# Kernel optimization log

Measured on AMD Instinct MI355X. Metric: run time of the kernel, lower is better.

## Reference

```python
import jax, jax.numpy as jnp
import numpy as np

HD = 256          # hidden_dim[0]
KF = 2            # k factor
KD = HD * KF      # 512, bilinear feature dim
L = 2000          # hard-coded sequence length
B = 4
NEG = np.float32(np.finfo(np.float32).min)  # finite min, NOT -inf (matches torch code)
EPS = 1e-5


def _fc(x, V, g, b):
    # weight_norm(Linear, dim=None): W = g * V / ||V||_F, then ReLU
    W = (g / jnp.linalg.norm(V)) * V  # [KD, HD]
    return jax.nn.relu(jnp.einsum('blh,kh->blk', x, W) + b)


def setup_inputs() -> dict:
    key = jax.random.key(0)
    ks = jax.random.split(key, 12)
    X = jax.random.normal(ks[0], (B, L, HD), dtype=jnp.float32)
    Y = jax.random.normal(ks[1], (B, L, HD), dtype=jnp.float32)
    mask1 = jax.random.bernoulli(ks[2], 0.8, (B, L)).astype(jnp.float32)
    mask2 = jax.random.bernoulli(ks[3], 0.8, (B, L)).astype(jnp.float32)
    # Q_net / K_net params (single weight-normed linear each)
    Qv = jax.random.normal(ks[4], (KD, HD), dtype=jnp.float32) * 0.05
    Qg = jnp.asarray(1.0, dtype=jnp.float32)
    Qb = jax.random.normal(ks[5], (KD,), dtype=jnp.float32) * 0.05
    Kv = jax.random.normal(ks[6], (KD, HD), dtype=jnp.float32) * 0.05
    Kg = jnp.asarray(1.0, dtype=jnp.float32)
    Kb = jax.random.normal(ks[7], (KD,), dtype=jnp.float32) * 0.05
    h_mat = jax.random.normal(ks[8], (KD,), dtype=jnp.float32)   # (1,1,KD) squeezed
    h_bias = jax.random.normal(ks[9], (), dtype=jnp.float32)     # (1,1,1) squeezed
    gamma = jnp.ones((KD,), dtype=jnp.float32)                   # BatchNorm1d affine
    beta = jnp.zeros((KD,), dtype=jnp.float32)
    return {"X": X, "Y": Y, "mask1": mask1, "mask2": mask2,
            "Qv": Qv, "Qg": Qg, "Qb": Qb, "Kv": Kv, "Kg": Kg, "Kb": Kb,
            "h_mat": h_mat, "h_bias": h_bias, "gamma": gamma, "beta": beta}


def _masked_softmax(A, m_row):
    # m_row: [B,1,L], broadcasts over axis 1; softmax over dim 1 as in torch
    logits = jnp.where(m_row > 0, A, NEG)
    att = jax.nn.softmax(logits, axis=1)
    return m_row * att


def reference(X, Y, mask1, mask2, Qv, Qg, Qb, Kv, Kg, Kb, h_mat, h_bias, gamma, beta):
    A1_X = _fc(X, Qv, Qg, Qb)  # [B,L,KD]
    A1_Y = _fc(Y, Kv, Kg, Kb)
    A2_Y = _fc(Y, Qv, Qg, Qb)
    A2_X = _fc(X, Kv, Kg, Kb)
    # bilinear co-attention maps [B,L,L]
    A1 = jnp.einsum('bvk,bqk->bvq', A1_X * h_mat, A1_Y) + h_bias
    A2 = jnp.einsum('bqk,bvk->bqv', A2_Y * h_mat, A2_X) + h_bias
    m1r = mask1[:, None, :]  # mask1_attend[b,v,q] = mask1[b,q]
    m2r = mask2[:, None, :]
    alpha = _masked_softmax(A1, m2r)
    logits_X = jnp.einsum('bvq,bqk->bvk', alpha, A1_Y) * mask1[:, :, None]
    beta_att = _masked_softmax(A2, m1r)
    logits_Y = jnp.einsum('bqv,bvk->bqk', beta_att, A2_X) * mask2[:, :, None]
    # AvgPool2d((2000,1)) == mean over sequence dim
    pooled = logits_X.mean(axis=1) + logits_Y.mean(axis=1)  # [B,KD]
    # BatchNorm1d training-mode forward (biased batch stats)
    mu = pooled.mean(axis=0)
    var = pooled.var(axis=0)
    return gamma * (pooled - mu) * jax.lax.rsqrt(var + EPS) + beta
```

## Files before the change

### kernel.cpp

```cpp
#include <hip/hip_runtime.h>

#define NB 4
#define LSEQ 2000
#define HD 256
#define KD 512
#define LPAD 2048
#define SMALL_N 18562

using short8 = __attribute__((ext_vector_type(8))) short;
using f32x4  = __attribute__((ext_vector_type(4))) float;
typedef unsigned short u16;

__device__ __forceinline__ float b2f(u16 u) { return __uint_as_float(((unsigned)u) << 16); }
__device__ __forceinline__ u16 f2b(float f) {
    unsigned u = __float_as_uint(f);
    u += 0x7FFFu + ((u >> 16) & 1u);
    return (u16)(u >> 16);
}
__device__ __forceinline__ bool detect32(const void* gamma) {
    return ((const float*)gamma)[0] == 1.0f;
}
__device__ __forceinline__ void gl_lds16(const u16* g, short* l) {
    __builtin_amdgcn_global_load_lds(
        (const __attribute__((address_space(1))) unsigned int*)g,
        (__attribute__((address_space(3))) unsigned int*)l, 16, 0, 0);
}

__global__ void convert_kernel(const void* X, const void* Y, const void* Qv, const void* Kv,
                               const void* m1, const void* m2, const void* Qb, const void* Kb,
                               const void* hm, const void* Qg, const void* Kg,
                               const void* gamma, const void* beta,
                               u16* __restrict__ Xb, u16* __restrict__ Yb,
                               u16* __restrict__ Qvb, u16* __restrict__ Kvb,
                               float* __restrict__ smallf, float* __restrict__ ssq)
{
    const bool is32 = detect32(gamma);
    const int seg = blockIdx.y;
    if (seg < 4) {
        const void* src = seg == 0 ? X : seg == 1 ? Y : seg == 2 ? Qv : Kv;
        u16* dst = seg == 0 ? Xb : seg == 1 ? Yb : seg == 2 ? Qvb : Kvb;
        const int n = (seg < 2) ? NB * LSEQ * HD : KD * HD;
        const int i0 = (blockIdx.x * 256 + threadIdx.x) * 8;
        if (i0 >= n) return;
        uint4 pack;
        u16* v = (u16*)&pack;
        if (is32) {
            float4 fa = ((const float4*)src)[(i0 >> 2)];
            float4 fb = ((const float4*)src)[(i0 >> 2) + 1];
            v[0] = f2b(fa.x); v[1] = f2b(fa.y); v[2] = f2b(fa.z); v[3] = f2b(fa.w);
            v[4] = f2b(fb.x); v[5] = f2b(fb.y); v[6] = f2b(fb.z); v[7] = f2b(fb.w);
        } else {
            pack = ((const uint4*)src)[i0 >> 3];
        }
        ((uint4*)dst)[i0 >> 3] = pack;
        if (seg >= 2) {
            float s = 0.f;
            #pragma unroll
            for (int j = 0; j < 8; ++j) { float f = b2f(v[j]); s = fmaf(f, f, s); }
            #pragma unroll
            for (int off = 32; off > 0; off >>= 1) s += __shfl_xor(s, off);
            if ((threadIdx.x & 63) == 0) atomicAdd(&ssq[seg - 2], s);
        }
    } else {
        const int i0 = (blockIdx.x * 256 + threadIdx.x) * 4;
        for (int i = i0; i < i0 + 4; ++i) {
            if (i >= SMALL_N) break;
            const void* src; int off;
            if      (i <  8000) { src = m1;    off = i; }
            else if (i < 16000) { src = m2;    off = i - 8000; }
            else if (i < 16512) { src = Qb;    off = i - 16000; }
            else if (i < 17024) { src = Kb;    off = i - 16512; }
            else if (i < 17536) { src = hm;    off = i - 17024; }
            else if (i < 18048) { src = gamma; off = i - 17536; }
            else if (i < 18560) { src = beta;  off = i - 18048; }
            else if (i == 18560) {
                float f = ((const float*)Qg)[0];
                smallf[i] = (f == 1.0f) ? 1.0f : b2f(((const u16*)Qg)[0]);
                continue;
            } else {
                float f = ((const float*)Kg)[0];
                smallf[i] = (f == 1.0f) ? 1.0f : b2f(((const u16*)Kg)[0]);
                continue;
            }
            smallf[i] = is32 ? ((const float*)src)[off] : b2f(((const u16*)src)[off]);
        }
    }
}

__global__ __launch_bounds__(256, 2)
void fc_kernel(const u16* __restrict__ X, const u16* __restrict__ Y,
               const u16* __restrict__ Qv, const u16* __restrict__ Kv,
               const float* __restrict__ Qbf, const float* __restrict__ Kbf,
               const float* __restrict__ hf, const float* __restrict__ gv,
               const float* __restrict__ ssq, u16* __restrict__ fc)
{
    const int mt = blockIdx.x, nt = blockIdx.y, t = blockIdx.z;
    const int b = t >> 2, which = t & 3;
    const u16* In = ((which == 0) | (which == 3)) ? (X + (size_t)b * LSEQ * HD)
                                                  : (Y + (size_t)b * LSEQ * HD);
    const bool isQ = (which == 0) | (which == 2);
    const u16* W      = isQ ? Qv : Kv;
    const float* bias = isQ ? Qbf : Kbf;
    const int j = isQ ? 0 : 1;
    const float s = gv[j] / sqrtf(ssq[j]);
    u16* out = fc + (size_t)t * LSEQ * KD;

    __shared__ __align__(16) short As[2][128 * 32];
    __shared__ __align__(16) short Bs[2][128 * 32];

    const int tid = threadIdx.x;
    const int lane = tid & 63, wave = tid >> 6;
    const int wm = wave >> 1, wn = wave & 1;
    const int quad = lane >> 4, l15 = lane & 15;
    const int sr = tid >> 2, sc = tid & 3;
    const int scz = sc ^ ((sr >> 1) & 3);
    const int m0 = mt * 128, n0 = nt * 128;

    int gm0 = min(m0 + sr, LSEQ - 1), gm1 = min(m0 + sr + 64, LSEQ - 1);
    const u16* pA0 = In + (size_t)gm0 * HD + scz * 8;
    const u16* pA1 = In + (size_t)gm1 * HD + scz * 8;
    const u16* pB0 = W + (size_t)(n0 + sr) * HD + scz * 8;
    const u16* pB1 = W + (size_t)(n0 + sr + 64) * HD + scz * 8;
    const int dof = sr * 32 + sc * 8;

    int aoff[4], boff[4];
    #pragma unroll
    for (int i = 0; i < 4; ++i) {
        int ra = wm * 64 + i * 16 + l15;
        aoff[i] = ra * 32 + (quad ^ ((ra >> 1) & 3)) * 8;
        int rb = wn * 64 + i * 16 + l15;
        boff[i] = rb * 32 + (quad ^ ((rb >> 1) & 3)) * 8;
    }

    gl_lds16(pA0, &As[0][dof]);
    gl_lds16(pA1, &As[0][64 * 32 + dof]);
    gl_lds16(pB0, &Bs[0][dof]);
    gl_lds16(pB1, &Bs[0][64 * 32 + dof]);
    __syncthreads();

    f32x4 acc[4][4] = {};

    for (int kt = 0; kt < 8; ++kt) {
        const int cur = kt & 1, nxt = cur ^ 1;
        if (kt < 7) {
            const int ko = (kt + 1) * 32;
            gl_lds16(pA0 + ko, &As[nxt][dof]);
            gl_lds16(pA1 + ko, &As[nxt][64 * 32 + dof]);
            gl_lds16(pB0 + ko, &Bs[nxt][dof]);
            gl_lds16(pB1 + ko, &Bs[nxt][64 * 32 + dof]);
        }
        short8 af[4], bf[4];
        #pragma unroll
        for (int i = 0; i < 4; ++i) af[i] = *(const short8*)&As[cur][aoff[i]];
        #pragma unroll
        for (int i = 0; i < 4; ++i) bf[i] = *(const short8*)&Bs[cur][boff[i]];
        #pragma unroll
        for (int mi = 0; mi < 4; ++mi)
            #pragma unroll
            for (int ni = 0; ni < 4; ++ni)
                acc[mi][ni] = __builtin_amdgcn_mfma_f32_16x16x32_bf16(af[mi], bf[ni], acc[mi][ni], 0, 0, 0);
        __syncthreads();
    }

    #pragma unroll
    for (int ni = 0; ni < 4; ++ni) {
        int n = n0 + wn * 64 + ni * 16 + l15;
        float bv = bias[n];
        float hv = isQ ? hf[n] : 1.0f;
        #pragma unroll
        for (int mi = 0; mi < 4; ++mi) {
            int mb = m0 + wm * 64 + mi * 16 + quad * 4;
            #pragma unroll
            for (int r = 0; r < 4; ++r) {
                int m = mb + r;
                if (m < LSEQ) {
                    float v = fmaf(s, acc[mi][ni][r], bv);
                    v = v > 0.f ? v : 0.f;
                    out[(size_t)m * KD + n] = f2b(v * hv);
                }
            }
        }
    }
}

__global__ __launch_bounds__(512, 2)
void colsm_kernel(const u16* __restrict__ fc, const float* __restrict__ m1f,
                  const float* __restrict__ m2f,
                  float* __restrict__ part_d, float* __restrict__ part_n)
{
    const int n_lin = blockIdx.x + 8 * blockIdx.y + 64 * blockIdx.z;
    const int xcd = n_lin & 7, slot = n_lin >> 3;
    const int pvs = xcd & 3, gqt = xcd >> 2;
    const int inner = slot & 7;
    const int vs = 2 * pvs + (inner & 1);
    const int qt = 4 * gqt + (inner >> 1);
    const int z  = slot >> 3;
    const int a = z >> 2, b = z & 3;
    const u16* R  = fc + (size_t)(b * 4 + (a == 0 ? 1 : 3)) * LSEQ * KD;
    const u16* Sm = fc + (size_t)(b * 4 + (a == 0 ? 0 : 2)) * LSEQ * KD;
    const float* wmask = (a == 0 ? m1f : m2f) + (size_t)b * LSEQ;

    __shared__ __align__(16) short AL[4][256 * 32];
    __shared__ __align__(16) short BL[4][256 * 32];

    const int tid = threadIdx.x;
    const int lane = tid & 63, wave = tid >> 6;
    const int wm = wave >> 2, wn = wave & 3;
    const int quad = lane >> 4, l15 = lane & 15;
    const int r0 = qt * 256, c0 = vs * 256;

    const int srow = tid >> 2;
    const int kslot = (tid & 3) ^ ((tid >> 3) & 3);
    int grA0 = min(r0 + srow, LSEQ - 1), grA1 = min(r0 + 128 + srow, LSEQ - 1);
    int gcB0 = min(c0 + srow, LSEQ - 1), gcB1 = min(c0 + 128 + srow, LSEQ - 1);
    const u16* pRa = R  + (size_t)grA0 * KD + kslot * 8;
    const u16* pRb = R  + (size_t)grA1 * KD + kslot * 8;
    const u16* pSa = Sm + (size_t)gcB0 * KD + kslot * 8;
    const u16* pSb = Sm + (size_t)gcB1 * KD + kslot * 8;
    const int ldst = tid * 8;

    const int swz = (quad ^ ((l15 >> 1) & 3)) * 8;

    #define STAGE_A(h) { short* d_ = &AL[(h) & 3][ldst];               \
                         gl_lds16(pRa + (h) * 32, d_);                 \
                         gl_lds16(pRb + (h) * 32, d_ + 4096); }
    #define STAGE_B(h) { short* d_ = &BL[(h) & 3][ldst];               \
                         gl_lds16(pSa + (h) * 32, d_);                 \
                         gl_lds16(pSb + (h) * 32, d_ + 4096); }

    STAGE_A(0); STAGE_B(0); STAGE_A(1); STAGE_B(1); STAGE_A(2); STAGE_B(2);
    asm volatile("s_waitcnt vmcnt(4)" ::: "memory");
    __builtin_amdgcn_s_barrier();
    __builtin_amdgcn_sched_barrier(0);

    f32x4 acc[8][4] = {};
    short8 bf[4];

    #pragma unroll 2
    for (int t = 0; t < 8; ++t) {
        #pragma unroll
        for (int p = 0; p < 4; ++p) {
            const int j = 2 * t + (p >> 1);
            const short* Ab = AL[j & 3];
            const short* Bb = BL[j & 3];
            short8 af[4];
            #pragma unroll
            for (int mi = 0; mi < 4; ++mi) {
                int lr = wm * 128 + (p & 1) * 64 + mi * 16 + l15;
                af[mi] = *(const short8*)&Ab[lr * 32 + swz];
            }
            if ((p & 1) == 0) {
                #pragma unroll
                for (int ni = 0; ni < 4; ++ni) {
                    int lc = wn * 64 + ni * 16 + l15;
                    bf[ni] = *(const short8*)&Bb[lc * 32 + swz];
                }
            }
            if (p == 0)      { if (2 * t + 3 <= 15) STAGE_A(2 * t + 3); }
            else if (p == 1) { if (2 * t + 3 <= 15) STAGE_B(2 * t + 3); }
            else if (p == 2) { if (2 * t + 4 <= 15) STAGE_A(2 * t + 4); }
            else {
                if (2 * t + 4 <= 15) STAGE_B(2 * t + 4);
                if (t < 6)       asm volatile("s_waitcnt vmcnt(4)" ::: "memory");
                else if (t == 6) asm volatile("s_waitcnt vmcnt(0)" ::: "memory");
            }
            asm volatile("" ::: "memory");
            __builtin_amdgcn_s_barrier();
            __builtin_amdgcn_sched_barrier(0);
            __builtin_amdgcn_s_setprio(1);
            #pragma unroll
            for (int mi = 0; mi < 4; ++mi)
                #pragma unroll
                for (int ni = 0; ni < 4; ++ni)
                    acc[(p & 1) * 4 + mi][ni] =
                        __builtin_amdgcn_mfma_f32_16x16x32_bf16(af[mi], bf[ni],
                                                                acc[(p & 1) * 4 + mi][ni], 0, 0, 0);
            __builtin_amdgcn_s_setprio(0);
            asm volatile("" ::: "memory");
            __builtin_amdgcn_s_barrier();
            __builtin_amdgcn_sched_barrier(0);
        }
    }

    __syncthreads();
    float* ldsD = (float*)&AL[0][0];
    float* ldsN = (float*)&AL[1][0];

    float wv[4], vv[4];
    #pragma unroll
    for (int ni = 0; ni < 4; ++ni) {
        int cg = c0 + wn * 64 + ni * 16 + l15;
        bool valid = cg < LSEQ;
        vv[ni] = valid ? 1.f : 0.f;
        wv[ni] = valid ? wmask[min(cg, LSEQ - 1)] : 0.f;
    }
    #pragma unroll
    for (int aq = 0; aq < 8; ++aq)
        #pragma unroll
        for (int r = 0; r < 4; ++r) {
            float d = 0.f, n = 0.f;
            #pragma unroll
            for (int ni = 0; ni < 4; ++ni) {
                float e = __expf(acc[aq][ni][r]);
                d = fmaf(vv[ni], e, d);
                n = fmaf(wv[ni], e, n);
            }
            #pragma unroll
            for (int off = 1; off < 16; off <<= 1) {
                d += __shfl_xor(d, off);
                n += __shfl_xor(n, off);
            }
            if (l15 == 0) {
                int row = wm * 128 + (aq >> 2) * 64 + (aq & 3) * 16 + quad * 4 + r;
                ldsD[row * 4 + wn] = d;
                ldsN[row * 4 + wn] = n;
            }
        }
    __syncthreads();
    if (tid < 256) {
        int q = r0 + tid;
        if (q < LSEQ) {
            size_t p = ((size_t)(z * 8 + vs)) * LPAD + q;
            part_d[p] = ldsD[tid * 4 + 0] + ldsD[tid * 4 + 1] + ldsD[tid * 4 + 2] + ldsD[tid * 4 + 3];
            part_n[p] = ldsN[tid * 4 + 0] + ldsN[tid * 4 + 1] + ldsN[tid * 4 + 2] + ldsN[tid * 4 + 3];
        }
    }
    #undef STAGE_A
    #undef STAGE_B
}

__global__ void combine_kernel(const float* __restrict__ part_d, const float* __restrict__ part_n,
                               const float* __restrict__ m1f, const float* __restrict__ m2f,
                               float* __restrict__ c, float* __restrict__ pooled)
{
    int idx = blockIdx.x * 256 + threadIdx.x;
    if (idx < NB * KD) pooled[idx] = 0.f;
    int z = idx >> 11, q = idx & (LPAD - 1);
    int a = z >> 2, b = z & 3;
    float d = 0.f, n = 0.f;
    #pragma unroll
    for (int vs = 0; vs < 8; ++vs) {
        size_t p = ((size_t)(z * 8 + vs)) * LPAD + q;
        d += part_d[p]; n += part_n[p];
    }
    float val = 0.f;
    if (q < LSEQ) {
        float om = (a == 0 ? m2f : m1f)[b * LSEQ + q];
        val = om * n / d;
    }
    c[(size_t)z * LPAD + q] = val;
}

__global__ void pooled_kernel(const u16* __restrict__ fc, const float* __restrict__ c,
                              float* __restrict__ pooled)
{
    const int b = blockIdx.x, rs = blockIdx.y;
    const int k = threadIdx.x;
    const u16* YK = fc + (size_t)(b * 4 + 1) * LSEQ * KD;
    const u16* XK = fc + (size_t)(b * 4 + 3) * LSEQ * KD;
    const float* c1 = c + (size_t)(0 + b) * LPAD;
    const float* c2 = c + (size_t)(4 + b) * LPAD;
    float s = 0.f;
    const int rbeg = rs * 50, rend = rbeg + 50;
    for (int r = rbeg; r < rend; ++r) {
        s = fmaf(c1[r], b2f(YK[(size_t)r * KD + k]), s);
        s = fmaf(c2[r], b2f(XK[(size_t)r * KD + k]), s);
    }
    atomicAdd(&pooled[b * KD + k], s * (1.0f / LSEQ));
}

__global__ void ln_kernel(const float* __restrict__ pooled, const float* __restrict__ gammaf,
                          const float* __restrict__ betaf, const void* __restrict__ gamma_orig,
                          void* __restrict__ out)
{
    int k = blockIdx.x * 256 + threadIdx.x;
    float p[NB];
    #pragma unroll
    for (int b = 0; b < NB; ++b) p[b] = pooled[b * KD + k];
    float mu = 0.25f * (p[0] + p[1] + p[2] + p[3]);
    float var = 0.f;
    #pragma unroll
    for (int b = 0; b < NB; ++b) { float d = p[b] - mu; var = fmaf(d, d, var); }
    var *= 0.25f;
    float inv = rsqrtf(var + 1e-5f);
    float g = gammaf[k], be = betaf[k];
    const bool is32 = detect32(gamma_orig);
    #pragma unroll
    for (int b = 0; b < NB; ++b) {
        float v = fmaf(g * (p[b] - mu), inv, be);
        if (is32) ((float*)out)[b * KD + k] = v;
        else      ((u16*)out)[b * KD + k] = f2b(v);
    }
}

extern "C" void kernel_launch(void* const* d_in, const int* in_sizes, int n_in,
                              void* d_out, int out_size, void* d_ws, size_t ws_size,
                              hipStream_t stream)
{
    const void* X  = d_in[0];
    const void* Y  = d_in[1];
    const void* m1 = d_in[2];
    const void* m2 = d_in[3];
    const void* Qv = d_in[4];
    const void* Qg = d_in[5];
    const void* Qb = d_in[6];
    const void* Kv = d_in[7];
    const void* Kg = d_in[8];
    const void* Kb = d_in[9];
    const void* h  = d_in[10];
    const void* gamma = d_in[12];
    const void* beta  = d_in[13];

    char* ws = (char*)d_ws;
    size_t off = 0;
    u16* Xb  = (u16*)(ws + off); off += (size_t)NB * LSEQ * HD * 2;
    u16* Yb  = (u16*)(ws + off); off += (size_t)NB * LSEQ * HD * 2;
    u16* Qvb = (u16*)(ws + off); off += (size_t)KD * HD * 2;
    u16* Kvb = (u16*)(ws + off); off += (size_t)KD * HD * 2;
    float* smallf = (float*)(ws + off); off += ((size_t)(SMALL_N + 2) * 4 + 15) / 16 * 16;
    u16* fc  = (u16*)(ws + off); off += (size_t)16 * LSEQ * KD * 2;
    float* part_d = (float*)(ws + off); off += (size_t)8 * 8 * LPAD * 4;
    float* part_n = (float*)(ws + off); off += (size_t)8 * 8 * LPAD * 4;
    float* c      = (float*)(ws + off); off += (size_t)8 * LPAD * 4;
    float* pooled = (float*)(ws + off); off += (size_t)NB * KD * 4;

    const float* m1f = smallf;
    const float* m2f = smallf + 8000;
    const float* Qbf = smallf + 16000;
    const float* Kbf = smallf + 16512;
    const float* hf  = smallf + 17024;
    const float* gmf = smallf + 17536;
    const float* bef = smallf + 18048;
    const float* gv  = smallf + 18560;
    float* ssq = smallf + SMALL_N;

    hipMemsetAsync(ssq, 0, 2 * sizeof(float), stream);
    convert_kernel<<<dim3(1000, 5), 256, 0, stream>>>(X, Y, Qv, Kv, m1, m2, Qb, Kb, h, Qg, Kg,
                                                      gamma, beta, Xb, Yb, Qvb, Kvb, smallf, ssq);
    fc_kernel     <<<dim3(16, 4, 16), 256, 0, stream>>>(Xb, Yb, Qvb, Kvb, Qbf, Kbf, hf, gv, ssq, fc);
    colsm_kernel  <<<dim3(8, 8, 8), 512, 0, stream>>>(fc, m1f, m2f, part_d, part_n);
    combine_kernel<<<64, 256, 0, stream>>>(part_d, part_n, m1f, m2f, c, pooled);
    pooled_kernel <<<dim3(4, 40), 512, 0, stream>>>(fc, c, pooled);
    ln_kernel     <<<2, 256, 0, stream>>>(pooled, gmf, bef, gamma, d_out);
}
```

Before: 188.5 us.

## Shrink colsm LDS ring to double buffer and raise occupancy bound

Replaces the 4-deep LDS staging ring and its hand-scheduled vmcnt waits and split barriers with a plain double buffer. Each iteration prefetches the next K slice and ends with a __syncthreads. Softmax reduction scratch moves to its own small shared arrays, and launch bounds rise from 2 to 4 blocks. The aim is to cut LDS use so more blocks fit per CU and latency is hidden by occupancy instead of deep prefetch. In exchange the register cap tightens a lot against a 128-float accumulator, which risks spills, and each step now pays a full barrier with a shallower prefetch.

```diff
diff --git a/kernel.cpp b/kernel.cpp
--- a/kernel.cpp
+++ b/kernel.cpp
@@ -183,7 +183,7 @@
     }
 }
 
-__global__ __launch_bounds__(512, 2)
+__global__ __launch_bounds__(512, 4)
 void colsm_kernel(const u16* __restrict__ fc, const float* __restrict__ m1f,
                   const float* __restrict__ m2f,
                   float* __restrict__ part_d, float* __restrict__ part_n)
@@ -200,8 +200,10 @@
     const u16* Sm = fc + (size_t)(b * 4 + (a == 0 ? 0 : 2)) * LSEQ * KD;
     const float* wmask = (a == 0 ? m1f : m2f) + (size_t)b * LSEQ;
 
-    __shared__ __align__(16) short AL[4][256 * 32];
-    __shared__ __align__(16) short BL[4][256 * 32];
+    __shared__ __align__(16) short AL[2][256 * 32];
+    __shared__ __align__(16) short BL[2][256 * 32];
+    __shared__ float ldsD[256][4];
+    __shared__ float ldsN[256][4];
 
     const int tid = threadIdx.x;
     const int lane = tid & 63, wave = tid >> 6;
@@ -218,73 +220,51 @@
     const u16* pSa = Sm + (size_t)gcB0 * KD + kslot * 8;
     const u16* pSb = Sm + (size_t)gcB1 * KD + kslot * 8;
     const int ldst = tid * 8;
-
     const int swz = (quad ^ ((l15 >> 1) & 3)) * 8;
 
-    #define STAGE_A(h) { short* d_ = &AL[(h) & 3][ldst];               \
-                         gl_lds16(pRa + (h) * 32, d_);                 \
-                         gl_lds16(pRb + (h) * 32, d_ + 4096); }
-    #define STAGE_B(h) { short* d_ = &BL[(h) & 3][ldst];               \
-                         gl_lds16(pSa + (h) * 32, d_);                 \
-                         gl_lds16(pSb + (h) * 32, d_ + 4096); }
-
-    STAGE_A(0); STAGE_B(0); STAGE_A(1); STAGE_B(1); STAGE_A(2); STAGE_B(2);
-    asm volatile("s_waitcnt vmcnt(4)" ::: "memory");
-    __builtin_amdgcn_s_barrier();
-    __builtin_amdgcn_sched_barrier(0);
+    #define STAGE_A(j) { short* d_ = &AL[(j) & 1][ldst];               \
+                         gl_lds16(pRa + (j) * 32, d_);                 \
+                         gl_lds16(pRb + (j) * 32, d_ + 4096); }
+    #define STAGE_B(j) { short* d_ = &BL[(j) & 1][ldst];               \
+                         gl_lds16(pSa + (j) * 32, d_);                 \
+                         gl_lds16(pSb + (j) * 32, d_ + 4096); }
+
+    STAGE_A(0); STAGE_B(0);
+    __syncthreads();
 
     f32x4 acc[8][4] = {};
-    short8 bf[4];
 
     #pragma unroll 2
-    for (int t = 0; t < 8; ++t) {
-        #pragma unroll
-        for (int p = 0; p < 4; ++p) {
-            const int j = 2 * t + (p >> 1);
-            const short* Ab = AL[j & 3];
-            const short* Bb = BL[j & 3];
+    for (int j = 0; j < 16; ++j) {
+        if (j < 15) { STAGE_A(j + 1); STAGE_B(j + 1); }
+        const short* Ab = AL[j & 1];
+        const short* Bb = BL[j & 1];
+        short8 bf[4];
+        #pragma unroll
+        for (int ni = 0; ni < 4; ++ni) {
+            int lc = wn * 64 + ni * 16 + l15;
+            bf[ni] = *(const short8*)&Bb[lc * 32 + swz];
+        }
+        #pragma unroll
+        for (int half = 0; half < 2; ++half) {
             short8 af[4];
             #pragma unroll
             for (int mi = 0; mi < 4; ++mi) {
-                int lr = wm * 128 + (p & 1) * 64 + mi * 16 + l15;
+                int lr = wm * 128 + half * 64 + mi * 16 + l15;
                 af[mi] = *(const short8*)&Ab[lr * 32 + swz];
             }
-            if ((p & 1) == 0) {
-                #pragma unroll
-                for (int ni = 0; ni < 4; ++ni) {
-                    int lc = wn * 64 + ni * 16 + l15;
-                    bf[ni] = *(const short8*)&Bb[lc * 32 + swz];
-                }
-            }
-            if (p == 0)      { if (2 * t + 3 <= 15) STAGE_A(2 * t + 3); }
-            else if (p == 1) { if (2 * t + 3 <= 15) STAGE_B(2 * t + 3); }
-            else if (p == 2) { if (2 * t + 4 <= 15) STAGE_A(2 * t + 4); }
-            else {
-                if (2 * t + 4 <= 15) STAGE_B(2 * t + 4);
-                if (t < 6)       asm volatile("s_waitcnt vmcnt(4)" ::: "memory");
-                else if (t == 6) asm volatile("s_waitcnt vmcnt(0)" ::: "memory");
-            }
-            asm volatile("" ::: "memory");
-            __builtin_amdgcn_s_barrier();
-            __builtin_amdgcn_sched_barrier(0);
             __builtin_amdgcn_s_setprio(1);
             #pragma unroll
             for (int mi = 0; mi < 4; ++mi)
                 #pragma unroll
                 for (int ni = 0; ni < 4; ++ni)
-                    acc[(p & 1) * 4 + mi][ni] =
+                    acc[half * 4 + mi][ni] =
                         __builtin_amdgcn_mfma_f32_16x16x32_bf16(af[mi], bf[ni],
-                                                                acc[(p & 1) * 4 + mi][ni], 0, 0, 0);
+                                                                acc[half * 4 + mi][ni], 0, 0, 0);
             __builtin_amdgcn_s_setprio(0);
-            asm volatile("" ::: "memory");
-            __builtin_amdgcn_s_barrier();
-            __builtin_amdgcn_sched_barrier(0);
-        }
-    }
-
-    __syncthreads();
-    float* ldsD = (float*)&AL[0][0];
-    float* ldsN = (float*)&AL[1][0];
+        }
+        __syncthreads();
+    }
 
     float wv[4], vv[4];
     #pragma unroll
@@ -312,8 +292,8 @@
             }
             if (l15 == 0) {
                 int row = wm * 128 + (aq >> 2) * 64 + (aq & 3) * 16 + quad * 4 + r;
-                ldsD[row * 4 + wn] = d;
-                ldsN[row * 4 + wn] = n;
+                ldsD[row][wn] = d;
+                ldsN[row][wn] = n;
             }
         }
     __syncthreads();
@@ -321,8 +301,8 @@
         int q = r0 + tid;
         if (q < LSEQ) {
             size_t p = ((size_t)(z * 8 + vs)) * LPAD + q;
-            part_d[p] = ldsD[tid * 4 + 0] + ldsD[tid * 4 + 1] + ldsD[tid * 4 + 2] + ldsD[tid * 4 + 3];
-            part_n[p] = ldsN[tid * 4 + 0] + ldsN[tid * 4 + 1] + ldsN[tid * 4 + 2] + ldsN[tid * 4 + 3];
+            part_d[p] = ldsD[tid][0] + ldsD[tid][1] + ldsD[tid][2] + ldsD[tid][3];
+            part_n[p] = ldsN[tid][0] + ldsN[tid][1] + ldsN[tid][2] + ldsN[tid][3];
         }
     }
     #undef STAGE_A
```

Measured after the change: 394.7 us. 109% more time.
